# Optimization experiments

Hardware: AMD Instinct MI355X
Metric: run time of the kernel (lower is better)

The kernel has to match this reference:

```python
import jax, jax.numpy as jnp
import numpy as np

TEMPERATURE = 0.07
NUM_NEGATIVES = 128
B, C, H, W = 4, 256, 32, 32
N_TOTAL = B * H * W  # 4096


def setup_inputs() -> dict:
    key = jax.random.key(0)
    k1, k2, k3 = jax.random.split(key, 3)
    feat_q = jax.random.normal(k1, (B, C, H, W), dtype=jnp.float32)
    feat_k = jax.random.normal(k2, (B, C, H, W), dtype=jnp.float32)
    # uniform draws in [0, N_TOTAL-1): same distribution as indexing into the
    # length-(N-1) 'choices' array in the original per-i loop
    neg_indices = jax.random.randint(k3, (N_TOTAL, NUM_NEGATIVES), 0, N_TOTAL - 1, dtype=jnp.int64 if jax.config.jax_enable_x64 else jnp.int32)
    return {"feat_q": feat_q, "feat_k": feat_k, "neg_indices": neg_indices}


def reference(feat_q, feat_k, neg_indices):
    b, c, h, w = feat_q.shape
    n = b * h * w
    q = feat_q.reshape(b, c, -1)
    k = feat_k.reshape(b, c, -1)
    # F.normalize(dim=1), eps=1e-12
    q = q / jnp.maximum(jnp.linalg.norm(q, axis=1, keepdims=True), 1e-12)
    k = k / jnp.maximum(jnp.linalg.norm(k, axis=1, keepdims=True), 1e-12)
    q = q.transpose(0, 2, 1).reshape(-1, c)  # [N, C]
    k = k.transpose(0, 2, 1).reshape(-1, c)  # [N, C]
    l_pos = jnp.sum(q * k, axis=1, keepdims=True)  # [N, 1]
    # self-exclusion: choices = all_idx without i -> shift sampled idx >= i up by 1
    row = jnp.arange(n, dtype=neg_indices.dtype)[:, None]
    idx = neg_indices + (neg_indices >= row).astype(neg_indices.dtype)  # [N, K]
    k_neg = k[idx]  # [N, K, C] gather
    l_neg = jnp.einsum('nc,nkc->nk', q, k_neg)  # [N, K]
    logits = jnp.concatenate([l_pos, l_neg], axis=1) / TEMPERATURE  # [N, 1+K]
    # cross-entropy with label 0 for every row
    loss = jnp.mean(jax.nn.logsumexp(logits, axis=1) - logits[:, 0])
    return loss
```

## Files before the change

kernel.cpp:

```cpp
#include <hip/hip_runtime.h>
#include <hip/hip_bf16.h>

#define N_TOTAL 4096
#define C_DIM 256
#define K_NEG 128
#define HW 1024
#define TEMP_INV (1.0f / 0.07f)

typedef _Float16 h8 __attribute__((ext_vector_type(8)));
typedef _Float16 h2 __attribute__((ext_vector_type(2)));

__global__ __launch_bounds__(256) void tr_ss_kernel(
    const float* __restrict__ fq, const float* __restrict__ fk,
    _Float16* __restrict__ qh, _Float16* __restrict__ kh,
    float* __restrict__ ss) {
  const int bid = blockIdx.x;
  const int tensor = bid >> 8;
  const int sp = (bid >> 2) & 63;
  const int cc = bid & 3;
  const float* in = tensor ? fk : fq;
  _Float16* out = tensor ? kh : qh;
  const int n0 = sp * 64;
  const int b = n0 / HW, s0 = n0 % HW;
  const float* base = in + (size_t)b * C_DIM * HW + s0;

  const int t = threadIdx.x, lane = t & 63, w = t >> 6;
  __shared__ float tile[64][65];
  __shared__ float red[4][64];

  const int chl = t >> 4;
  const int sp4 = (t & 15) * 4;
#pragma unroll
  for (int p = 0; p < 4; ++p) {
    int cl = p * 16 + chl;
    const float4 v =
        *(const float4*)(base + (size_t)(cc * 64 + cl) * HW + sp4);
    tile[cl][sp4] = v.x; tile[cl][sp4 + 1] = v.y;
    tile[cl][sp4 + 2] = v.z; tile[cl][sp4 + 3] = v.w;
  }
  __syncthreads();

  float acc = 0.f;
#pragma unroll
  for (int j = 0; j < 16; ++j) {
    float v = tile[w * 16 + j][lane];
    acc = fmaf(v, v, acc);
  }
  red[w][lane] = acc;
  __syncthreads();
  if (w == 0) {
    float tot = red[0][lane] + red[1][lane] + red[2][lane] + red[3][lane];
    atomicAdd(&ss[tensor * N_TOTAL + n0 + lane], tot);
  }

  const int wsp = t >> 2, q4 = t & 3;
  h8 o0, o1;
#pragma unroll
  for (int j = 0; j < 8; ++j) o0[j] = (_Float16)tile[q4 * 16 + j][wsp];
#pragma unroll
  for (int j = 0; j < 8; ++j) o1[j] = (_Float16)tile[q4 * 16 + 8 + j][wsp];
  h8* dst = (h8*)(out + (size_t)(n0 + wsp) * C_DIM + cc * 64 + q4 * 16);
  dst[0] = o0;
  dst[1] = o1;
}

__global__ __launch_bounds__(256) void nce_kernel(
    const _Float16* __restrict__ qh, const _Float16* __restrict__ kh,
    const float* __restrict__ ss, const int* __restrict__ neg,
    float* __restrict__ loss_buf) {
  const int n = blockIdx.x;
  const int t = threadIdx.x;
  const int lane = t & 63;
  const int w = t >> 6;
  const int sub = lane & 7;
  const int unit = w * 8 + (lane >> 3);

  __shared__ float sneg[K_NEG];
  __shared__ float s_lpos;

  const float* ssk_arr = ss + N_TOTAL;

  int r[4];
#pragma unroll
  for (int j = 0; j < 4; ++j) {
    int x = neg[(size_t)n * K_NEG + j * 32 + unit];
    r[j] = x + (x >= n ? 1 : 0);
  }
  const h8* qrow = (const h8*)(qh + (size_t)n * C_DIM);
  h8 qv[4];
#pragma unroll
  for (int i = 0; i < 4; ++i) qv[i] = qrow[i * 8 + sub];
  float ssq = ss[n];
  h8 kp[4];
  float sskp = 1.f;
  if (unit == 0) {
    const h8* kr = (const h8*)(kh + (size_t)n * C_DIM);
#pragma unroll
    for (int i = 0; i < 4; ++i) kp[i] = kr[i * 8 + sub];
    sskp = ssk_arr[n];
  }
  h8 kd[4][4];
  float ssk[4];
#pragma unroll
  for (int j = 0; j < 4; ++j) {
    const h8* kr = (const h8*)(kh + (size_t)r[j] * C_DIM);
#pragma unroll
    for (int i = 0; i < 4; ++i) kd[j][i] = kr[i * 8 + sub];
    ssk[j] = ssk_arr[r[j]];
  }
  __builtin_amdgcn_sched_barrier(0);

  const float invq = 1.0f / fmaxf(sqrtf(ssq), 1e-12f);

  union H { h8 v; h2 p[4]; };

#pragma unroll
  for (int j = 0; j < 4; ++j) {
    float a0 = 0.f, a1 = 0.f;
#pragma unroll
    for (int i = 0; i < 4; ++i) {
      H a; a.v = qv[i];
      H b; b.v = kd[j][i];
      a0 = __builtin_amdgcn_fdot2(b.p[0], a.p[0], a0, false);
      a1 = __builtin_amdgcn_fdot2(b.p[1], a.p[1], a1, false);
      a0 = __builtin_amdgcn_fdot2(b.p[2], a.p[2], a0, false);
      a1 = __builtin_amdgcn_fdot2(b.p[3], a.p[3], a1, false);
    }
    float acc = a0 + a1;
    acc += __shfl_xor(acc, 1);
    acc += __shfl_xor(acc, 2);
    acc += __shfl_xor(acc, 4);
    if (sub == 0) {
      float invk = 1.0f / fmaxf(sqrtf(ssk[j]), 1e-12f);
      sneg[j * 32 + unit] = acc * invq * invk;
    }
  }
  if (unit == 0) {
    float a0 = 0.f, a1 = 0.f;
#pragma unroll
    for (int i = 0; i < 4; ++i) {
      H a; a.v = qv[i];
      H b; b.v = kp[i];
      a0 = __builtin_amdgcn_fdot2(b.p[0], a.p[0], a0, false);
      a1 = __builtin_amdgcn_fdot2(b.p[1], a.p[1], a1, false);
      a0 = __builtin_amdgcn_fdot2(b.p[2], a.p[2], a0, false);
      a1 = __builtin_amdgcn_fdot2(b.p[3], a.p[3], a1, false);
    }
    float acc = a0 + a1;
    acc += __shfl_xor(acc, 1);
    acc += __shfl_xor(acc, 2);
    acc += __shfl_xor(acc, 4);
    if (sub == 0) {
      float invk = 1.0f / fmaxf(sqrtf(sskp), 1e-12f);
      s_lpos = acc * invq * invk;
    }
  }
  __syncthreads();

  if (w == 0) {
    float lp = s_lpos * TEMP_INV;
    float x1 = sneg[lane] * TEMP_INV;
    float x2 = sneg[lane + 64] * TEMP_INV;
    float m = fmaxf(fmaxf(x1, x2), lp);
#pragma unroll
    for (int off = 32; off; off >>= 1) m = fmaxf(m, __shfl_xor(m, off));
    float s = __expf(x1 - m) + __expf(x2 - m);
#pragma unroll
    for (int off = 32; off; off >>= 1) s += __shfl_xor(s, off);
    if (lane == 0) loss_buf[n] = m + __logf(s) - lp;
  }
}

__global__ __launch_bounds__(1024) void reduce_kernel(
    const float* __restrict__ loss_buf, float* __restrict__ out) {
  const int t = threadIdx.x;
  const float4 v = ((const float4*)loss_buf)[t];
  float s = (v.x + v.y) + (v.z + v.w);
#pragma unroll
  for (int off = 32; off; off >>= 1) s += __shfl_xor(s, off);
  __shared__ float red[16];
  if ((t & 63) == 0) red[t >> 6] = s;
  __syncthreads();
  if (t < 16) {
    float x = red[t];
#pragma unroll
    for (int off = 8; off; off >>= 1) x += __shfl_xor(x, off);
    if (t == 0) out[0] = x * (1.0f / N_TOTAL);
  }
}

extern "C" void kernel_launch(void* const* d_in, const int* in_sizes, int n_in,
                              void* d_out, int out_size, void* d_ws,
                              size_t ws_size, hipStream_t stream) {
  const float* fq = (const float*)d_in[0];
  const float* fk = (const float*)d_in[1];
  const int* neg = (const int*)d_in[2];
  float* out = (float*)d_out;

  _Float16* qh = (_Float16*)d_ws;
  _Float16* kh = qh + (size_t)N_TOTAL * C_DIM;
  float* ss = (float*)(kh + (size_t)N_TOTAL * C_DIM);
  float* loss_buf = ss + 2 * N_TOTAL;

  hipMemsetAsync(ss, 0, 2 * N_TOTAL * sizeof(float), stream);
  hipLaunchKernelGGL(tr_ss_kernel, dim3(512), dim3(256), 0, stream,
                     fq, fk, qh, kh, ss);
  hipLaunchKernelGGL(nce_kernel, dim3(N_TOTAL), dim3(256), 0, stream,
                     qh, kh, ss, neg, loss_buf);
  hipLaunchKernelGGL(reduce_kernel, dim3(1), dim3(1024), 0, stream,
                     loss_buf, out);
}
```

Measured before the change: 84.69 us.

## Stage gathered negative key rows into LDS via direct global-to-LDS loads

Replaces per-thread register gathers of negative key rows with global_load_lds DMA transfers that copy all 128 gathered fp16 rows (64 KB) into shared memory, then computes dot products reading from LDS. Inverse key norms are precomputed once per negative into shared memory. This aims to issue wide coalesced 512-byte row loads and cut VGPR pressure. The cost is 64 KB of LDS per block, which sharply limits occupancy and latency hiding, plus a full wait and barrier before any compute.

```diff
diff --git a/kernel.cpp b/kernel.cpp
--- a/kernel.cpp
+++ b/kernel.cpp
@@ -9,6 +9,12 @@
 
 typedef _Float16 h8 __attribute__((ext_vector_type(8)));
 typedef _Float16 h2 __attribute__((ext_vector_type(2)));
+
+__device__ __forceinline__ void lds_dma16(const void* g, void* l) {
+  __builtin_amdgcn_global_load_lds(
+      (const __attribute__((address_space(1))) void*)g,
+      (__attribute__((address_space(3))) void*)l, 16, 0, 0);
+}
 
 __global__ __launch_bounds__(256) void tr_ss_kernel(
     const float* __restrict__ fq, const float* __restrict__ fk,
@@ -73,54 +79,59 @@
   const int lane = t & 63;
   const int w = t >> 6;
   const int sub = lane & 7;
-  const int unit = w * 8 + (lane >> 3);
-
+  const int unit = lane >> 3;
+
+  __shared__ __align__(16) _Float16 krows[K_NEG][C_DIM];
+  __shared__ float sinvk[K_NEG];
   __shared__ float sneg[K_NEG];
   __shared__ float s_lpos;
 
   const float* ssk_arr = ss + N_TOTAL;
 
-  int r[4];
-#pragma unroll
-  for (int j = 0; j < 4; ++j) {
-    int x = neg[(size_t)n * K_NEG + j * 32 + unit];
-    r[j] = x + (x >= n ? 1 : 0);
-  }
   const h8* qrow = (const h8*)(qh + (size_t)n * C_DIM);
   h8 qv[4];
 #pragma unroll
   for (int i = 0; i < 4; ++i) qv[i] = qrow[i * 8 + sub];
   float ssq = ss[n];
+
   h8 kp[4];
   float sskp = 1.f;
-  if (unit == 0) {
+  if (t < 8) {
     const h8* kr = (const h8*)(kh + (size_t)n * C_DIM);
 #pragma unroll
     for (int i = 0; i < 4; ++i) kp[i] = kr[i * 8 + sub];
     sskp = ssk_arr[n];
   }
-  h8 kd[4][4];
-  float ssk[4];
-#pragma unroll
-  for (int j = 0; j < 4; ++j) {
-    const h8* kr = (const h8*)(kh + (size_t)r[j] * C_DIM);
-#pragma unroll
-    for (int i = 0; i < 4; ++i) kd[j][i] = kr[i * 8 + sub];
-    ssk[j] = ssk_arr[r[j]];
-  }
-  __builtin_amdgcn_sched_barrier(0);
+
+  int myidx = 0;
+  if (lane < 32) {
+    int x = neg[(size_t)n * K_NEG + w * 32 + lane];
+    myidx = x + (x >= n ? 1 : 0);
+    sinvk[w * 32 + lane] = 1.0f / fmaxf(sqrtf(ssk_arr[myidx]), 1e-12f);
+  }
+
+#pragma unroll
+  for (int j = 0; j < 16; ++j) {
+    int r0 = __shfl(myidx, 2 * j + (lane >> 5));
+    const char* src =
+        (const char*)(kh + (size_t)r0 * C_DIM) + (lane & 31) * 16;
+    lds_dma16(src, &krows[w * 32 + 2 * j][0]);
+  }
+  asm volatile("s_waitcnt vmcnt(0) lgkmcnt(0)" ::: "memory");
+  __syncthreads();
 
   const float invq = 1.0f / fmaxf(sqrtf(ssq), 1e-12f);
-
   union H { h8 v; h2 p[4]; };
 
 #pragma unroll
-  for (int j = 0; j < 4; ++j) {
+  for (int jj = 0; jj < 4; ++jj) {
+    const int rr = w * 32 + unit * 4 + jj;
+    const h8* kr = (const h8*)&krows[rr][0];
     float a0 = 0.f, a1 = 0.f;
 #pragma unroll
     for (int i = 0; i < 4; ++i) {
       H a; a.v = qv[i];
-      H b; b.v = kd[j][i];
+      H b; b.v = kr[i * 8 + sub];
       a0 = __builtin_amdgcn_fdot2(b.p[0], a.p[0], a0, false);
       a1 = __builtin_amdgcn_fdot2(b.p[1], a.p[1], a1, false);
       a0 = __builtin_amdgcn_fdot2(b.p[2], a.p[2], a0, false);
@@ -130,12 +141,10 @@
     acc += __shfl_xor(acc, 1);
     acc += __shfl_xor(acc, 2);
     acc += __shfl_xor(acc, 4);
-    if (sub == 0) {
-      float invk = 1.0f / fmaxf(sqrtf(ssk[j]), 1e-12f);
-      sneg[j * 32 + unit] = acc * invq * invk;
-    }
-  }
-  if (unit == 0) {
+    if (sub == 0) sneg[rr] = acc * invq * sinvk[rr];
+  }
+
+  if (t < 8) {
     float a0 = 0.f, a1 = 0.f;
 #pragma unroll
     for (int i = 0; i < 4; ++i) {
@@ -150,10 +159,7 @@
     acc += __shfl_xor(acc, 1);
     acc += __shfl_xor(acc, 2);
     acc += __shfl_xor(acc, 4);
-    if (sub == 0) {
-      float invk = 1.0f / fmaxf(sqrtf(sskp), 1e-12f);
-      s_lpos = acc * invq * invk;
-    }
+    if (t == 0) s_lpos = acc * invq * (1.0f / fmaxf(sqrtf(sskp), 1e-12f));
   }
   __syncthreads();
 
```

New measurement: 104.0 us. 1.23x slower.

## Normalize features in transpose kernel and drop sum-of-squares buffer and memset

Applied to the files above, without the earlier changes.

The transpose kernel now gives each block 16 spatial positions across all 256 channels, so it can compute the full L2 norm locally and write pre-normalized fp16 vectors. The temperature factor is folded into q. This removes the memset, the atomics and the per-neighbor norm loads in the NCE kernel. The cost is a less coalesced read pattern (16 contiguous floats per channel row) and storing scaled q at fp16, which shifts precision slightly.

```diff
diff --git a/kernel.cpp b/kernel.cpp
--- a/kernel.cpp
+++ b/kernel.cpp
@@ -10,64 +10,74 @@
 typedef _Float16 h8 __attribute__((ext_vector_type(8)));
 typedef _Float16 h2 __attribute__((ext_vector_type(2)));
 
-__global__ __launch_bounds__(256) void tr_ss_kernel(
+__global__ __launch_bounds__(256) void norm_tr_kernel(
     const float* __restrict__ fq, const float* __restrict__ fk,
-    _Float16* __restrict__ qh, _Float16* __restrict__ kh,
-    float* __restrict__ ss) {
+    _Float16* __restrict__ qh, _Float16* __restrict__ kh) {
   const int bid = blockIdx.x;
   const int tensor = bid >> 8;
-  const int sp = (bid >> 2) & 63;
-  const int cc = bid & 3;
-  const float* in = tensor ? fk : fq;
+  const int chunk = bid & 255;
+  const int n0 = chunk * 16;
+  const int b = n0 / HW, s0 = n0 % HW;
+  const float* base = (tensor ? fk : fq) + (size_t)b * C_DIM * HW + s0;
   _Float16* out = tensor ? kh : qh;
-  const int n0 = sp * 64;
-  const int b = n0 / HW, s0 = n0 % HW;
-  const float* base = in + (size_t)b * C_DIM * HW + s0;
-
-  const int t = threadIdx.x, lane = t & 63, w = t >> 6;
-  __shared__ float tile[64][65];
-  __shared__ float red[4][64];
-
-  const int chl = t >> 4;
-  const int sp4 = (t & 15) * 4;
-#pragma unroll
-  for (int p = 0; p < 4; ++p) {
-    int cl = p * 16 + chl;
-    const float4 v =
-        *(const float4*)(base + (size_t)(cc * 64 + cl) * HW + sp4);
-    tile[cl][sp4] = v.x; tile[cl][sp4 + 1] = v.y;
-    tile[cl][sp4 + 2] = v.z; tile[cl][sp4 + 3] = v.w;
-  }
-  __syncthreads();
-
-  float acc = 0.f;
-#pragma unroll
-  for (int j = 0; j < 16; ++j) {
-    float v = tile[w * 16 + j][lane];
-    acc = fmaf(v, v, acc);
-  }
-  red[w][lane] = acc;
-  __syncthreads();
-  if (w == 0) {
-    float tot = red[0][lane] + red[1][lane] + red[2][lane] + red[3][lane];
-    atomicAdd(&ss[tensor * N_TOTAL + n0 + lane], tot);
-  }
-
-  const int wsp = t >> 2, q4 = t & 3;
-  h8 o0, o1;
-#pragma unroll
-  for (int j = 0; j < 8; ++j) o0[j] = (_Float16)tile[q4 * 16 + j][wsp];
-#pragma unroll
-  for (int j = 0; j < 8; ++j) o1[j] = (_Float16)tile[q4 * 16 + 8 + j][wsp];
-  h8* dst = (h8*)(out + (size_t)(n0 + wsp) * C_DIM + cc * 64 + q4 * 16);
-  dst[0] = o0;
-  dst[1] = o1;
+  const float scale_extra = tensor ? 1.0f : TEMP_INV;
+
+  const int t = threadIdx.x;
+  __shared__ float tile[16][C_DIM + 1];
+  __shared__ float red[16][17];
+  __shared__ float sinv[16];
+
+  {
+    const int c = t;
+    const float* src = base + (size_t)c * HW;
+#pragma unroll
+    for (int p = 0; p < 4; ++p) {
+      const float4 v = *(const float4*)(src + p * 4);
+      tile[p * 4 + 0][c] = v.x;
+      tile[p * 4 + 1][c] = v.y;
+      tile[p * 4 + 2][c] = v.z;
+      tile[p * 4 + 3][c] = v.w;
+    }
+  }
+  __syncthreads();
+
+  {
+    const int s = t & 15, cg = t >> 4;
+    float acc = 0.f;
+#pragma unroll
+    for (int i = 0; i < 16; ++i) {
+      float v = tile[s][cg * 16 + i];
+      acc = fmaf(v, v, acc);
+    }
+    red[s][cg] = acc;
+  }
+  __syncthreads();
+  if (t < 16) {
+    float tot = 0.f;
+#pragma unroll
+    for (int g = 0; g < 16; ++g) tot += red[t][g];
+    sinv[t] = scale_extra / fmaxf(sqrtf(tot), 1e-12f);
+  }
+  __syncthreads();
+
+  {
+    const int s = t & 15, c16 = t >> 4;
+    const float inv = sinv[s];
+    h8 o0, o1;
+#pragma unroll
+    for (int j = 0; j < 8; ++j) o0[j] = (_Float16)(tile[s][c16 * 16 + j] * inv);
+#pragma unroll
+    for (int j = 0; j < 8; ++j)
+      o1[j] = (_Float16)(tile[s][c16 * 16 + 8 + j] * inv);
+    h8* dst = (h8*)(out + (size_t)(n0 + s) * C_DIM + c16 * 16);
+    dst[0] = o0;
+    dst[1] = o1;
+  }
 }
 
 __global__ __launch_bounds__(256) void nce_kernel(
     const _Float16* __restrict__ qh, const _Float16* __restrict__ kh,
-    const float* __restrict__ ss, const int* __restrict__ neg,
-    float* __restrict__ loss_buf) {
+    const int* __restrict__ neg, float* __restrict__ loss_buf) {
   const int n = blockIdx.x;
   const int t = threadIdx.x;
   const int lane = t & 63;
@@ -78,8 +88,6 @@
   __shared__ float sneg[K_NEG];
   __shared__ float s_lpos;
 
-  const float* ssk_arr = ss + N_TOTAL;
-
   int r[4];
 #pragma unroll
   for (int j = 0; j < 4; ++j) {
@@ -90,27 +98,20 @@
   h8 qv[4];
 #pragma unroll
   for (int i = 0; i < 4; ++i) qv[i] = qrow[i * 8 + sub];
-  float ssq = ss[n];
   h8 kp[4];
-  float sskp = 1.f;
   if (unit == 0) {
     const h8* kr = (const h8*)(kh + (size_t)n * C_DIM);
 #pragma unroll
     for (int i = 0; i < 4; ++i) kp[i] = kr[i * 8 + sub];
-    sskp = ssk_arr[n];
   }
   h8 kd[4][4];
-  float ssk[4];
 #pragma unroll
   for (int j = 0; j < 4; ++j) {
     const h8* kr = (const h8*)(kh + (size_t)r[j] * C_DIM);
 #pragma unroll
     for (int i = 0; i < 4; ++i) kd[j][i] = kr[i * 8 + sub];
-    ssk[j] = ssk_arr[r[j]];
   }
   __builtin_amdgcn_sched_barrier(0);
-
-  const float invq = 1.0f / fmaxf(sqrtf(ssq), 1e-12f);
 
   union H { h8 v; h2 p[4]; };
 
@@ -130,10 +131,7 @@
     acc += __shfl_xor(acc, 1);
     acc += __shfl_xor(acc, 2);
     acc += __shfl_xor(acc, 4);
-    if (sub == 0) {
-      float invk = 1.0f / fmaxf(sqrtf(ssk[j]), 1e-12f);
-      sneg[j * 32 + unit] = acc * invq * invk;
-    }
+    if (sub == 0) sneg[j * 32 + unit] = acc;
   }
   if (unit == 0) {
     float a0 = 0.f, a1 = 0.f;
@@ -150,17 +148,14 @@
     acc += __shfl_xor(acc, 1);
     acc += __shfl_xor(acc, 2);
     acc += __shfl_xor(acc, 4);
-    if (sub == 0) {
-      float invk = 1.0f / fmaxf(sqrtf(sskp), 1e-12f);
-      s_lpos = acc * invq * invk;
-    }
+    if (sub == 0) s_lpos = acc;
   }
   __syncthreads();
 
   if (w == 0) {
-    float lp = s_lpos * TEMP_INV;
-    float x1 = sneg[lane] * TEMP_INV;
-    float x2 = sneg[lane + 64] * TEMP_INV;
+    float lp = s_lpos;
+    float x1 = sneg[lane];
+    float x2 = sneg[lane + 64];
     float m = fmaxf(fmaxf(x1, x2), lp);
 #pragma unroll
     for (int off = 32; off; off >>= 1) m = fmaxf(m, __shfl_xor(m, off));
@@ -199,14 +194,12 @@
 
   _Float16* qh = (_Float16*)d_ws;
   _Float16* kh = qh + (size_t)N_TOTAL * C_DIM;
-  float* ss = (float*)(kh + (size_t)N_TOTAL * C_DIM);
-  float* loss_buf = ss + 2 * N_TOTAL;
-
-  hipMemsetAsync(ss, 0, 2 * N_TOTAL * sizeof(float), stream);
-  hipLaunchKernelGGL(tr_ss_kernel, dim3(512), dim3(256), 0, stream,
-                     fq, fk, qh, kh, ss);
+  float* loss_buf = (float*)(kh + (size_t)N_TOTAL * C_DIM);
+
+  hipLaunchKernelGGL(norm_tr_kernel, dim3(512), dim3(256), 0, stream,
+                     fq, fk, qh, kh);
   hipLaunchKernelGGL(nce_kernel, dim3(N_TOTAL), dim3(256), 0, stream,
-                     qh, kh, ss, neg, loss_buf);
+                     qh, kh, neg, loss_buf);
   hipLaunchKernelGGL(reduce_kernel, dim3(1), dim3(1024), 0, stream,
                      loss_buf, out);
 }
```

Result: faster. 82.41 us (-2.7%).
